# Kernel tuning notes

Measured on AMD Instinct MI355X. Metric: run time of the kernel, lower is better.

The kernel has to match this reference:

```python
import jax, jax.numpy as jnp
import numpy as np
from jax import lax

B = 4096
PRO_VOCAB, PRO_LEN, PRO_K = 25, 1000, 8
LIG_VOCAB, LIG_LEN, LIG_K = 64, 100, 4
CH = 96  # 2*CH = 192 = 6*32 per the reshape in the original forward
DN = ('NCH', 'OIH', 'NCH')  # 1D conv dimension numbers


def setup_inputs() -> dict:
    key = jax.random.key(0)
    ks = jax.random.split(key, 8)
    protein = jax.random.normal(ks[0], (B, PRO_VOCAB, PRO_LEN), dtype=jnp.float32)
    ligand = jax.random.normal(ks[1], (B, LIG_VOCAB, LIG_LEN), dtype=jnp.float32)
    w_pro = jax.random.normal(ks[2], (CH, PRO_VOCAB, PRO_K), dtype=jnp.float32) * 0.05
    b_pro = jnp.zeros((CH,), dtype=jnp.float32)
    w_lig = jax.random.normal(ks[3], (CH, LIG_VOCAB, LIG_K), dtype=jnp.float32) * 0.05
    b_lig = jnp.zeros((CH,), dtype=jnp.float32)
    # QuLinear readout over the 32*32=1024 amplitude-encoded Gram matrix -> scalar
    w_aff = jax.random.normal(ks[4], (1024,), dtype=jnp.float32) * 0.05
    b_aff = jnp.zeros((), dtype=jnp.float32)
    return {"protein": protein, "ligand": ligand, "w_pro": w_pro, "b_pro": b_pro,
            "w_lig": w_lig, "b_lig": b_lig, "w_aff": w_aff, "b_aff": b_aff}


def _conv_branch(x, w, b):
    # Conv1d (valid) -> ReLU -> global max pool over length  =>  (B, CH)
    y = lax.conv_general_dilated(x, w, (1,), 'VALID', dimension_numbers=DN)
    return jnp.max(jax.nn.relu(y + b[None, :, None]), axis=-1)


def reference(protein, ligand, w_pro, b_pro, w_lig, b_lig, w_aff, b_aff):
    x1 = _conv_branch(ligand, w_lig, b_lig)    # (B, 96)
    x2 = _conv_branch(protein, w_pro, b_pro)   # (B, 96)
    x = jnp.concatenate([x1, x2], axis=1).reshape(-1, 6, 32)  # (B, 6, 32)
    # Vectorized per-sample Gram matrix a.T @ a : (B, 32, 32)
    gram = jnp.einsum('bij,bik->bjk', x, x)
    flat = gram.reshape(gram.shape[0], -1)     # (B, 1024)
    # Amplitude encoding: L2-normalize the flattened Gram matrix per sample
    amp = flat / (jnp.linalg.norm(flat, axis=1, keepdims=True) + 1e-12)
    # QuLinear readout -> scalar affinity per sample
    aff = amp @ w_aff + b_aff                  # (B,)
    return aff
```

## Files before the change

### kernel.cpp

```cpp
#include <hip/hip_runtime.h>
#include <math.h>

typedef _Float16 f16;
typedef _Float16 f16x2 __attribute__((ext_vector_type(2)));
typedef _Float16 f16x8 __attribute__((ext_vector_type(8)));
typedef float f32x4 __attribute__((ext_vector_type(4)));

__global__ void repack_pro_kernel(const float* __restrict__ w, f16* __restrict__ wp) {
    constexpr int V = 25, K = 8;
    int i = blockIdx.x * 256 + threadIdx.x;
    if (i >= K * 6 * 64 * 8) return;
    int e = i & 7, l = (i >> 3) & 63, c6 = (i >> 9) % 6, t = i / (512 * 6);
    int r16 = l & 15, g = l >> 4;
    int ch = c6 * 16 + r16, v = g * 8 + e;
    float val = (v < V) ? w[(ch * V + v) * K + t] : 0.f;
    wp[i] = (f16)val;
}

__global__ void repack_lig_kernel(const float* __restrict__ w, f16* __restrict__ wp) {
    constexpr int V = 64, K = 4;
    int i = blockIdx.x * 256 + threadIdx.x;
    if (i >= 8 * 6 * 64 * 8) return;
    int e = i & 7, l = (i >> 3) & 63, c6 = (i >> 9) % 6, tk = i / (512 * 6);
    int t = tk >> 1, ks = tk & 1;
    int r16 = l & 15, g = l >> 4;
    int ch = c6 * 16 + r16, v = ks * 32 + g * 8 + e;
    wp[i] = (f16)w[(ch * V + v) * K + t];
}

__global__ __launch_bounds__(512, 4) void conv_kernel(
    const float* __restrict__ pro,
    const f16*   __restrict__ wpP,
    const float* __restrict__ bP,
    const float* __restrict__ lig,
    const f16*   __restrict__ wpL,
    const float* __restrict__ bL,
    float* __restrict__ feat,
    int B)
{
    __shared__ __align__(16) char s_raw[264 * 80];
    __shared__ __align__(16) f16  s_w[24576];
    __shared__ float s_red[8 * 96];

    const int tid  = threadIdx.x;
    const int wave = tid >> 6;
    const int lane = tid & 63;
    const int g    = lane >> 4;
    const int r16  = lane & 15;

    if ((int)blockIdx.x < B) {
        constexpr int V = 25, L = 1000, KT = 8, LOUT = 993;
        constexpr int CH = 256, NC = 4, BR = 264, RSB = 80;
        constexpr int P4 = BR / 4, NVP = 13, NU = NVP * P4;
        const size_t b = blockIdx.x;
        const float* gs = pro + b * (size_t)(V * L);

        {   const f16x8* wg = (const f16x8*)wpP;
            f16x8* wl = (f16x8*)s_w;
            #pragma unroll
            for (int u = 0; u < 24576 / 8 / 512; ++u)
                wl[u * 512 + tid] = wg[u * 512 + tid];
        }
        for (int row = tid; row < BR; row += 512) {
            const int swz = ((row >> 3) & 3) << 4;
            *(f16x8*)(s_raw + row * RSB + (48 ^ swz)) = (f16x8){};
        }
        __syncthreads();

        float runmax[6];
        #pragma unroll
        for (int c6 = 0; c6 < 6; ++c6) runmax[c6] = -3.0e38f;

        for (int c = 0; c < NC; ++c) {
            if (c) __syncthreads();
            #pragma unroll
            for (int u = 0; u < 2; ++u) {
                const int i = u * 512 + tid;
                if (i < NU) {
                    const int v2 = i / P4, p4 = i - v2 * P4;
                    const int p  = 4 * p4;
                    const int gp = c * CH + p;
                    float4 x0 = {0.f, 0.f, 0.f, 0.f}, x1 = {0.f, 0.f, 0.f, 0.f};
                    if (gp < L) {
                        x0 = *(const float4*)(gs + (size_t)(2 * v2) * L + gp);
                        if (2 * v2 + 1 < V)
                            x1 = *(const float4*)(gs + (size_t)(2 * v2 + 1) * L + gp);
                    }
                    const int pb = 4 * v2;
                    const int slot = pb & 48, sub = pb & 12;
                    const float vx0[4] = {x0.x, x0.y, x0.z, x0.w};
                    const float vx1[4] = {x1.x, x1.y, x1.z, x1.w};
                    #pragma unroll
                    for (int j = 0; j < 4; ++j) {
                        const int row = p + j;
                        const int swz = ((row >> 3) & 3) << 4;
                        f16x2 hv = { (f16)vx0[j], (f16)vx1[j] };
                        *(f16x2*)(s_raw + row * RSB + ((slot ^ swz) + sub)) = hv;
                    }
                }
            }
            __syncthreads();

            f32x4 acc[2][6] = {};
            #pragma unroll 1
            for (int t = 0; t < KT; ++t) {
                f16x8 bf[6];
                #pragma unroll
                for (int c6 = 0; c6 < 6; ++c6)
                    bf[c6] = *(const f16x8*)(s_w + ((t * 6 + c6) * 64 + lane) * 8);
                #pragma unroll
                for (int rt = 0; rt < 2; ++rt) {
                    const int row = wave * 32 + rt * 16 + r16 + t;
                    const int swz = ((row >> 3) & 3) << 4;
                    f16x8 a = *(const f16x8*)(s_raw + row * RSB + ((g * 16) ^ swz));
                    #pragma unroll
                    for (int c6 = 0; c6 < 6; ++c6)
                        acc[rt][c6] = __builtin_amdgcn_mfma_f32_16x16x32_f16(a, bf[c6], acc[rt][c6], 0, 0, 0);
                }
            }
            #pragma unroll
            for (int rt = 0; rt < 2; ++rt) {
                const int pt = c * CH + wave * 32 + rt * 16;
                if (pt + 16 <= LOUT) {
                    #pragma unroll
                    for (int c6 = 0; c6 < 6; ++c6)
                        #pragma unroll
                        for (int i = 0; i < 4; ++i)
                            runmax[c6] = fmaxf(runmax[c6], acc[rt][c6][i]);
                } else {
                    const int p0g = pt + g * 4;
                    #pragma unroll
                    for (int c6 = 0; c6 < 6; ++c6)
                        #pragma unroll
                        for (int i = 0; i < 4; ++i)
                            if (p0g + i < LOUT) runmax[c6] = fmaxf(runmax[c6], acc[rt][c6][i]);
                }
            }
        }

        #pragma unroll
        for (int c6 = 0; c6 < 6; ++c6) {
            runmax[c6] = fmaxf(runmax[c6], __shfl_xor(runmax[c6], 16, 64));
            runmax[c6] = fmaxf(runmax[c6], __shfl_xor(runmax[c6], 32, 64));
        }
        if (lane < 16) {
            #pragma unroll
            for (int c6 = 0; c6 < 6; ++c6)
                s_red[wave * 96 + c6 * 16 + lane] = runmax[c6];
        }
        __syncthreads();
        if (tid < 96) {
            float m = s_red[tid];
            #pragma unroll
            for (int w = 1; w < 8; ++w) m = fmaxf(m, s_red[w * 96 + tid]);
            feat[b * 192 + 96 + tid] = fmaxf(m + bP[tid], 0.f);
        }
    } else {
        constexpr int V = 64, L = 100, KT = 4, LOUT = 97;
        constexpr int BR = 120, RSB = 144;
        constexpr int P4 = BR / 4, NVP = 32, NU = NVP * P4;
        const size_t b = blockIdx.x - B;
        const float* gs = lig + b * (size_t)(V * L);

        {   const f16x8* wg = (const f16x8*)wpL;
            f16x8* wl = (f16x8*)s_w;
            #pragma unroll
            for (int u = 0; u < 24576 / 8 / 512; ++u)
                wl[u * 512 + tid] = wg[u * 512 + tid];
        }
        #pragma unroll
        for (int u = 0; u < 2; ++u) {
            const int i = u * 512 + tid;
            if (i < NU) {
                const int v2 = i / P4, p4 = i - v2 * P4;
                const int p  = 4 * p4;
                float4 x0 = {0.f, 0.f, 0.f, 0.f}, x1 = {0.f, 0.f, 0.f, 0.f};
                if (p < L) {
                    x0 = *(const float4*)(gs + (size_t)(2 * v2) * L + p);
                    x1 = *(const float4*)(gs + (size_t)(2 * v2 + 1) * L + p);
                }
                const int pb = 4 * v2;
                const int slot = pb & 0x70, sub = pb & 12;
                const float vx0[4] = {x0.x, x0.y, x0.z, x0.w};
                const float vx1[4] = {x1.x, x1.y, x1.z, x1.w};
                #pragma unroll
                for (int j = 0; j < 4; ++j) {
                    const int row = p + j;
                    const int swz = ((row >> 3) & 3) << 4;
                    f16x2 hv = { (f16)vx0[j], (f16)vx1[j] };
                    *(f16x2*)(s_raw + row * RSB + ((slot ^ swz) + sub)) = hv;
                }
            }
        }
        __syncthreads();

        if (wave < 7) {
            f32x4 acc[6] = {};
            #pragma unroll 1
            for (int t = 0; t < KT; ++t) {
                #pragma unroll
                for (int ks = 0; ks < 2; ++ks) {
                    f16x8 bf[6];
                    #pragma unroll
                    for (int c6 = 0; c6 < 6; ++c6)
                        bf[c6] = *(const f16x8*)(s_w + (((t * 2 + ks) * 6 + c6) * 64 + lane) * 8);
                    const int row = wave * 16 + r16 + t;
                    const int swz = ((row >> 3) & 3) << 4;
                    f16x8 a = *(const f16x8*)(s_raw + row * RSB + ((ks * 64 + g * 16) ^ swz));
                    #pragma unroll
                    for (int c6 = 0; c6 < 6; ++c6)
                        acc[c6] = __builtin_amdgcn_mfma_f32_16x16x32_f16(a, bf[c6], acc[c6], 0, 0, 0);
                }
            }
            float runmax[6];
            const int p0g = wave * 16 + g * 4;
            #pragma unroll
            for (int c6 = 0; c6 < 6; ++c6) {
                runmax[c6] = -3.0e38f;
                #pragma unroll
                for (int i = 0; i < 4; ++i)
                    if (p0g + i < LOUT) runmax[c6] = fmaxf(runmax[c6], acc[c6][i]);
                runmax[c6] = fmaxf(runmax[c6], __shfl_xor(runmax[c6], 16, 64));
                runmax[c6] = fmaxf(runmax[c6], __shfl_xor(runmax[c6], 32, 64));
            }
            if (lane < 16) {
                #pragma unroll
                for (int c6 = 0; c6 < 6; ++c6)
                    s_red[wave * 96 + c6 * 16 + lane] = runmax[c6];
            }
        }
        __syncthreads();
        if (tid < 96) {
            float m = s_red[tid];
            #pragma unroll
            for (int w = 1; w < 7; ++w) m = fmaxf(m, s_red[w * 96 + tid]);
            feat[b * 192 + tid] = fmaxf(m + bL[tid], 0.f);
        }
    }
}

__global__ __launch_bounds__(256) void gram_affinity_kernel(
    const float* __restrict__ feat, const float* __restrict__ w_aff,
    const float* __restrict__ b_aff, float* __restrict__ out, int B)
{
    const int lane = threadIdx.x & 63;
    const int wid  = threadIdx.x >> 6;
    const int b    = blockIdx.x * 4 + wid;

    __shared__ float s_x[4][192];

    if (b < B) {
        const float* fp = feat + (size_t)b * 192;
        for (int i = lane; i < 192; i += 64) s_x[wid][i] = fp[i];
    }
    __syncthreads();

    if (b < B) {
        float ssum = 0.f, sdot = 0.f;
        #pragma unroll
        for (int t = 0; t < 16; ++t) {
            const int jk = t * 64 + lane;
            const int j = jk >> 5, k = jk & 31;
            float gg = 0.f;
            #pragma unroll
            for (int i = 0; i < 6; ++i)
                gg = fmaf(s_x[wid][i * 32 + j], s_x[wid][i * 32 + k], gg);
            ssum = fmaf(gg, gg, ssum);
            sdot = fmaf(gg, w_aff[jk], sdot);
        }
        #pragma unroll
        for (int off = 32; off >= 1; off >>= 1) {
            ssum += __shfl_xor(ssum, off, 64);
            sdot += __shfl_xor(sdot, off, 64);
        }
        if (lane == 0) out[b] = sdot / (sqrtf(ssum) + 1e-12f) + b_aff[0];
    }
}

extern "C" void kernel_launch(void* const* d_in, const int* in_sizes, int n_in,
                              void* d_out, int out_size, void* d_ws, size_t ws_size,
                              hipStream_t stream)
{
    const float* protein = (const float*)d_in[0];
    const float* ligand  = (const float*)d_in[1];
    const float* w_pro   = (const float*)d_in[2];
    const float* b_pro   = (const float*)d_in[3];
    const float* w_lig   = (const float*)d_in[4];
    const float* b_lig   = (const float*)d_in[5];
    const float* w_aff   = (const float*)d_in[6];
    const float* b_aff   = (const float*)d_in[7];
    float* out = (float*)d_out;
    const int B = out_size;

    float* feat   = (float*)d_ws;
    f16*   wpackP = (f16*)((char*)d_ws + (size_t)B * 192 * 4);
    f16*   wpackL = wpackP + 24576;

    repack_pro_kernel<<<96, 256, 0, stream>>>(w_pro, wpackP);
    repack_lig_kernel<<<96, 256, 0, stream>>>(w_lig, wpackL);

    conv_kernel<<<2 * B, 512, 0, stream>>>(
        protein, wpackP, b_pro, ligand, wpackL, b_lig, feat, B);

    gram_affinity_kernel<<<(B + 3) / 4, 256, 0, stream>>>(feat, w_aff, b_aff, out, B);
}
```

Measured before the change: 249.4 us.

## Stage whole protein sequence in LDS with 1024-thread blocks

Replaces the four-chunk protein loop with a single pass: blocks grow to 1024 threads (16 waves), the full 1032-row fp16 protein tile is staged into LDS at once, and each wave computes four 16-row MFMA tiles. This removes the per-chunk barriers and the repeated staging/compute alternation. In exchange, LDS use per block rises to roughly 133 KB and register pressure per wave grows, which limits blocks per CU. The ligand half, which needs only 7 waves, now launches with 1024 threads, so most of those threads sit idle.

```diff
diff --git a/kernel.cpp b/kernel.cpp
--- a/kernel.cpp
+++ b/kernel.cpp
@@ -28,7 +28,7 @@
     wp[i] = (f16)w[(ch * V + v) * K + t];
 }
 
-__global__ __launch_bounds__(512, 4) void conv_kernel(
+__global__ __launch_bounds__(1024) void conv_kernel(
     const float* __restrict__ pro,
     const f16*   __restrict__ wpP,
     const float* __restrict__ bP,
@@ -38,9 +38,9 @@
     float* __restrict__ feat,
     int B)
 {
-    __shared__ __align__(16) char s_raw[264 * 80];
+    __shared__ __align__(16) char s_raw[1032 * 80];
     __shared__ __align__(16) f16  s_w[24576];
-    __shared__ float s_red[8 * 96];
+    __shared__ float s_red[16 * 96];
 
     const int tid  = threadIdx.x;
     const int wave = tid >> 6;
@@ -50,137 +50,38 @@
 
     if ((int)blockIdx.x < B) {
         constexpr int V = 25, L = 1000, KT = 8, LOUT = 993;
-        constexpr int CH = 256, NC = 4, BR = 264, RSB = 80;
-        constexpr int P4 = BR / 4, NVP = 13, NU = NVP * P4;
+        constexpr int BR = 1032, RSB = 80;
+        constexpr int P4 = BR / 4;
+        constexpr int NU = 13 * P4;
         const size_t b = blockIdx.x;
         const float* gs = pro + b * (size_t)(V * L);
 
         {   const f16x8* wg = (const f16x8*)wpP;
             f16x8* wl = (f16x8*)s_w;
             #pragma unroll
-            for (int u = 0; u < 24576 / 8 / 512; ++u)
-                wl[u * 512 + tid] = wg[u * 512 + tid];
-        }
-        for (int row = tid; row < BR; row += 512) {
+            for (int u = 0; u < 3; ++u)
+                wl[u * 1024 + tid] = wg[u * 1024 + tid];
+        }
+        for (int row = tid; row < BR; row += 1024) {
             const int swz = ((row >> 3) & 3) << 4;
             *(f16x8*)(s_raw + row * RSB + (48 ^ swz)) = (f16x8){};
         }
         __syncthreads();
 
-        float runmax[6];
-        #pragma unroll
-        for (int c6 = 0; c6 < 6; ++c6) runmax[c6] = -3.0e38f;
-
-        for (int c = 0; c < NC; ++c) {
-            if (c) __syncthreads();
-            #pragma unroll
-            for (int u = 0; u < 2; ++u) {
-                const int i = u * 512 + tid;
-                if (i < NU) {
-                    const int v2 = i / P4, p4 = i - v2 * P4;
-                    const int p  = 4 * p4;
-                    const int gp = c * CH + p;
-                    float4 x0 = {0.f, 0.f, 0.f, 0.f}, x1 = {0.f, 0.f, 0.f, 0.f};
-                    if (gp < L) {
-                        x0 = *(const float4*)(gs + (size_t)(2 * v2) * L + gp);
-                        if (2 * v2 + 1 < V)
-                            x1 = *(const float4*)(gs + (size_t)(2 * v2 + 1) * L + gp);
-                    }
-                    const int pb = 4 * v2;
-                    const int slot = pb & 48, sub = pb & 12;
-                    const float vx0[4] = {x0.x, x0.y, x0.z, x0.w};
-                    const float vx1[4] = {x1.x, x1.y, x1.z, x1.w};
-                    #pragma unroll
-                    for (int j = 0; j < 4; ++j) {
-                        const int row = p + j;
-                        const int swz = ((row >> 3) & 3) << 4;
-                        f16x2 hv = { (f16)vx0[j], (f16)vx1[j] };
-                        *(f16x2*)(s_raw + row * RSB + ((slot ^ swz) + sub)) = hv;
-                    }
-                }
-            }
-            __syncthreads();
-
-            f32x4 acc[2][6] = {};
-            #pragma unroll 1
-            for (int t = 0; t < KT; ++t) {
-                f16x8 bf[6];
-                #pragma unroll
-                for (int c6 = 0; c6 < 6; ++c6)
-                    bf[c6] = *(const f16x8*)(s_w + ((t * 6 + c6) * 64 + lane) * 8);
-                #pragma unroll
-                for (int rt = 0; rt < 2; ++rt) {
-                    const int row = wave * 32 + rt * 16 + r16 + t;
-                    const int swz = ((row >> 3) & 3) << 4;
-                    f16x8 a = *(const f16x8*)(s_raw + row * RSB + ((g * 16) ^ swz));
-                    #pragma unroll
-                    for (int c6 = 0; c6 < 6; ++c6)
-                        acc[rt][c6] = __builtin_amdgcn_mfma_f32_16x16x32_f16(a, bf[c6], acc[rt][c6], 0, 0, 0);
-                }
-            }
-            #pragma unroll
-            for (int rt = 0; rt < 2; ++rt) {
-                const int pt = c * CH + wave * 32 + rt * 16;
-                if (pt + 16 <= LOUT) {
-                    #pragma unroll
-                    for (int c6 = 0; c6 < 6; ++c6)
-                        #pragma unroll
-                        for (int i = 0; i < 4; ++i)
-                            runmax[c6] = fmaxf(runmax[c6], acc[rt][c6][i]);
-                } else {
-                    const int p0g = pt + g * 4;
-                    #pragma unroll
-                    for (int c6 = 0; c6 < 6; ++c6)
-                        #pragma unroll
-                        for (int i = 0; i < 4; ++i)
-                            if (p0g + i < LOUT) runmax[c6] = fmaxf(runmax[c6], acc[rt][c6][i]);
-                }
-            }
-        }
-
-        #pragma unroll
-        for (int c6 = 0; c6 < 6; ++c6) {
-            runmax[c6] = fmaxf(runmax[c6], __shfl_xor(runmax[c6], 16, 64));
-            runmax[c6] = fmaxf(runmax[c6], __shfl_xor(runmax[c6], 32, 64));
-        }
-        if (lane < 16) {
-            #pragma unroll
-            for (int c6 = 0; c6 < 6; ++c6)
-                s_red[wave * 96 + c6 * 16 + lane] = runmax[c6];
-        }
-        __syncthreads();
-        if (tid < 96) {
-            float m = s_red[tid];
-            #pragma unroll
-            for (int w = 1; w < 8; ++w) m = fmaxf(m, s_red[w * 96 + tid]);
-            feat[b * 192 + 96 + tid] = fmaxf(m + bP[tid], 0.f);
-        }
-    } else {
-        constexpr int V = 64, L = 100, KT = 4, LOUT = 97;
-        constexpr int BR = 120, RSB = 144;
-        constexpr int P4 = BR / 4, NVP = 32, NU = NVP * P4;
-        const size_t b = blockIdx.x - B;
-        const float* gs = lig + b * (size_t)(V * L);
-
-        {   const f16x8* wg = (const f16x8*)wpL;
-            f16x8* wl = (f16x8*)s_w;
-            #pragma unroll
-            for (int u = 0; u < 24576 / 8 / 512; ++u)
-                wl[u * 512 + tid] = wg[u * 512 + tid];
-        }
-        #pragma unroll
-        for (int u = 0; u < 2; ++u) {
-            const int i = u * 512 + tid;
+        #pragma unroll
+        for (int u = 0; u < 4; ++u) {
+            const int i = u * 1024 + tid;
             if (i < NU) {
                 const int v2 = i / P4, p4 = i - v2 * P4;
                 const int p  = 4 * p4;
                 float4 x0 = {0.f, 0.f, 0.f, 0.f}, x1 = {0.f, 0.f, 0.f, 0.f};
                 if (p < L) {
                     x0 = *(const float4*)(gs + (size_t)(2 * v2) * L + p);
-                    x1 = *(const float4*)(gs + (size_t)(2 * v2 + 1) * L + p);
+                    if (2 * v2 + 1 < V)
+                        x1 = *(const float4*)(gs + (size_t)(2 * v2 + 1) * L + p);
                 }
                 const int pb = 4 * v2;
-                const int slot = pb & 0x70, sub = pb & 12;
+                const int slot = pb & 48, sub = pb & 12;
                 const float vx0[4] = {x0.x, x0.y, x0.z, x0.w};
                 const float vx1[4] = {x1.x, x1.y, x1.z, x1.w};
                 #pragma unroll
@@ -190,6 +91,98 @@
                     f16x2 hv = { (f16)vx0[j], (f16)vx1[j] };
                     *(f16x2*)(s_raw + row * RSB + ((slot ^ swz) + sub)) = hv;
                 }
+            }
+        }
+        __syncthreads();
+
+        float runmax[6];
+        #pragma unroll
+        for (int c6 = 0; c6 < 6; ++c6) runmax[c6] = -3.0e38f;
+
+        f32x4 acc[4][6] = {};
+        #pragma unroll 1
+        for (int t = 0; t < KT; ++t) {
+            f16x8 bf[6];
+            #pragma unroll
+            for (int c6 = 0; c6 < 6; ++c6)
+                bf[c6] = *(const f16x8*)(s_w + ((t * 6 + c6) * 64 + lane) * 8);
+            #pragma unroll
+            for (int rt = 0; rt < 4; ++rt) {
+                const int row = wave * 64 + rt * 16 + r16 + t;
+                const int swz = ((row >> 3) & 3) << 4;
+                f16x8 a = *(const f16x8*)(s_raw + row * RSB + ((g * 16) ^ swz));
+                #pragma unroll
+                for (int c6 = 0; c6 < 6; ++c6)
+                    acc[rt][c6] = __builtin_amdgcn_mfma_f32_16x16x32_f16(a, bf[c6], acc[rt][c6], 0, 0, 0);
+            }
+        }
+        #pragma unroll
+        for (int rt = 0; rt < 4; ++rt) {
+            const int pt = wave * 64 + rt * 16;
+            if (pt + 16 <= LOUT) {
+                #pragma unroll
+                for (int c6 = 0; c6 < 6; ++c6)
+                    #pragma unroll
+                    for (int i = 0; i < 4; ++i)
+                        runmax[c6] = fmaxf(runmax[c6], acc[rt][c6][i]);
+            } else {
+                const int p0g = pt + g * 4;
+                #pragma unroll
+                for (int c6 = 0; c6 < 6; ++c6)
+                    #pragma unroll
+                    for (int i = 0; i < 4; ++i)
+                        if (p0g + i < LOUT) runmax[c6] = fmaxf(runmax[c6], acc[rt][c6][i]);
+            }
+        }
+
+        #pragma unroll
+        for (int c6 = 0; c6 < 6; ++c6) {
+            runmax[c6] = fmaxf(runmax[c6], __shfl_xor(runmax[c6], 16, 64));
+            runmax[c6] = fmaxf(runmax[c6], __shfl_xor(runmax[c6], 32, 64));
+        }
+        if (lane < 16) {
+            #pragma unroll
+            for (int c6 = 0; c6 < 6; ++c6)
+                s_red[wave * 96 + c6 * 16 + lane] = runmax[c6];
+        }
+        __syncthreads();
+        if (tid < 96) {
+            float m = s_red[tid];
+            #pragma unroll
+            for (int w = 1; w < 16; ++w) m = fmaxf(m, s_red[w * 96 + tid]);
+            feat[b * 192 + 96 + tid] = fmaxf(m + bP[tid], 0.f);
+        }
+    } else {
+        constexpr int V = 64, L = 100, KT = 4, LOUT = 97;
+        constexpr int BR = 120, RSB = 144;
+        constexpr int P4 = BR / 4, NU = 32 * P4;
+        const size_t b = blockIdx.x - B;
+        const float* gs = lig + b * (size_t)(V * L);
+
+        {   const f16x8* wg = (const f16x8*)wpL;
+            f16x8* wl = (f16x8*)s_w;
+            #pragma unroll
+            for (int u = 0; u < 3; ++u)
+                wl[u * 1024 + tid] = wg[u * 1024 + tid];
+        }
+        if (tid < NU) {
+            const int v2 = tid / P4, p4 = tid - v2 * P4;
+            const int p  = 4 * p4;
+            float4 x0 = {0.f, 0.f, 0.f, 0.f}, x1 = {0.f, 0.f, 0.f, 0.f};
+            if (p < L) {
+                x0 = *(const float4*)(gs + (size_t)(2 * v2) * L + p);
+                x1 = *(const float4*)(gs + (size_t)(2 * v2 + 1) * L + p);
+            }
+            const int pb = 4 * v2;
+            const int slot = pb & 0x70, sub = pb & 12;
+            const float vx0[4] = {x0.x, x0.y, x0.z, x0.w};
+            const float vx1[4] = {x1.x, x1.y, x1.z, x1.w};
+            #pragma unroll
+            for (int j = 0; j < 4; ++j) {
+                const int row = p + j;
+                const int swz = ((row >> 3) & 3) << 4;
+                f16x2 hv = { (f16)vx0[j], (f16)vx1[j] };
+                *(f16x2*)(s_raw + row * RSB + ((slot ^ swz) + sub)) = hv;
             }
         }
         __syncthreads();
@@ -299,7 +292,7 @@
     repack_pro_kernel<<<96, 256, 0, stream>>>(w_pro, wpackP);
     repack_lig_kernel<<<96, 256, 0, stream>>>(w_lig, wpackL);
 
-    conv_kernel<<<2 * B, 512, 0, stream>>>(
+    conv_kernel<<<2 * B, 1024, 0, stream>>>(
         protein, wpackP, b_pro, ligand, wpackL, b_lig, feat, B);
 
     gram_affinity_kernel<<<(B + 3) / 4, 256, 0, stream>>>(feat, w_aff, b_aff, out, B);
```

Result: slower. 422.5 us (+69.4%).

## Split protein conv MFMA tile across row and channel waves, widen staging loads

Applied to the files above, without the earlier changes.

The protein branch now uses a 4x2 wave grid: each wave covers 64 output positions and 3 of the 6 channel groups, instead of 32 positions and all 6 groups. This halves the B-fragment loads per wave and doubles the reuse of each A fragment, while keeping the same number of MFMAs per wave. Input staging also changes so each thread loads four vocab rows at once and writes f16x4 to LDS, using one pass of 462 threads instead of two passes of 858 items. The cross-wave max reduction is adjusted to match the new split.

```diff
diff --git a/kernel.cpp b/kernel.cpp
--- a/kernel.cpp
+++ b/kernel.cpp
@@ -3,6 +3,7 @@
 
 typedef _Float16 f16;
 typedef _Float16 f16x2 __attribute__((ext_vector_type(2)));
+typedef _Float16 f16x4 __attribute__((ext_vector_type(4)));
 typedef _Float16 f16x8 __attribute__((ext_vector_type(8)));
 typedef float f32x4 __attribute__((ext_vector_type(4)));
 
@@ -51,9 +52,11 @@
     if ((int)blockIdx.x < B) {
         constexpr int V = 25, L = 1000, KT = 8, LOUT = 993;
         constexpr int CH = 256, NC = 4, BR = 264, RSB = 80;
-        constexpr int P4 = BR / 4, NVP = 13, NU = NVP * P4;
+        constexpr int P4 = BR / 4;
+        constexpr int NU = 7 * P4;
         const size_t b = blockIdx.x;
         const float* gs = pro + b * (size_t)(V * L);
+        const int rw = wave & 3, cw = wave >> 2;
 
         {   const f16x8* wg = (const f16x8*)wpP;
             f16x8* wl = (f16x8*)s_w;
@@ -67,98 +70,101 @@
         }
         __syncthreads();
 
-        float runmax[6];
-        #pragma unroll
-        for (int c6 = 0; c6 < 6; ++c6) runmax[c6] = -3.0e38f;
+        float runmax[3];
+        #pragma unroll
+        for (int c3 = 0; c3 < 3; ++c3) runmax[c3] = -3.0e38f;
 
         for (int c = 0; c < NC; ++c) {
             if (c) __syncthreads();
-            #pragma unroll
-            for (int u = 0; u < 2; ++u) {
-                const int i = u * 512 + tid;
-                if (i < NU) {
-                    const int v2 = i / P4, p4 = i - v2 * P4;
-                    const int p  = 4 * p4;
-                    const int gp = c * CH + p;
-                    float4 x0 = {0.f, 0.f, 0.f, 0.f}, x1 = {0.f, 0.f, 0.f, 0.f};
-                    if (gp < L) {
-                        x0 = *(const float4*)(gs + (size_t)(2 * v2) * L + gp);
-                        if (2 * v2 + 1 < V)
-                            x1 = *(const float4*)(gs + (size_t)(2 * v2 + 1) * L + gp);
+            if (tid < NU) {
+                const int vq = tid / P4, p4 = tid - vq * P4;
+                const int p = 4 * p4, gp = c * CH + p;
+                float4 x0 = {0.f,0.f,0.f,0.f}, x1 = {0.f,0.f,0.f,0.f};
+                float4 x2 = {0.f,0.f,0.f,0.f}, x3 = {0.f,0.f,0.f,0.f};
+                if (gp < L) {
+                    x0 = *(const float4*)(gs + (size_t)(4 * vq) * L + gp);
+                    if (vq < 6) {
+                        x1 = *(const float4*)(gs + (size_t)(4 * vq + 1) * L + gp);
+                        x2 = *(const float4*)(gs + (size_t)(4 * vq + 2) * L + gp);
+                        x3 = *(const float4*)(gs + (size_t)(4 * vq + 3) * L + gp);
                     }
-                    const int pb = 4 * v2;
-                    const int slot = pb & 48, sub = pb & 12;
-                    const float vx0[4] = {x0.x, x0.y, x0.z, x0.w};
-                    const float vx1[4] = {x1.x, x1.y, x1.z, x1.w};
-                    #pragma unroll
-                    for (int j = 0; j < 4; ++j) {
-                        const int row = p + j;
-                        const int swz = ((row >> 3) & 3) << 4;
-                        f16x2 hv = { (f16)vx0[j], (f16)vx1[j] };
-                        *(f16x2*)(s_raw + row * RSB + ((slot ^ swz) + sub)) = hv;
-                    }
+                }
+                const int pb = 8 * vq;
+                const int slot = pb & 48, sub = pb & 8;
+                const float a0[4] = {x0.x, x0.y, x0.z, x0.w};
+                const float a1[4] = {x1.x, x1.y, x1.z, x1.w};
+                const float a2[4] = {x2.x, x2.y, x2.z, x2.w};
+                const float a3[4] = {x3.x, x3.y, x3.z, x3.w};
+                #pragma unroll
+                for (int j = 0; j < 4; ++j) {
+                    const int row = p + j;
+                    const int swz = ((row >> 3) & 3) << 4;
+                    f16x4 hv = { (f16)a0[j], (f16)a1[j], (f16)a2[j], (f16)a3[j] };
+                    *(f16x4*)(s_raw + row * RSB + ((slot ^ swz) + sub)) = hv;
                 }
             }
             __syncthreads();
 
-            f32x4 acc[2][6] = {};
+            f32x4 acc[4][3] = {};
             #pragma unroll 1
             for (int t = 0; t < KT; ++t) {
-                f16x8 bf[6];
-                #pragma unroll
-                for (int c6 = 0; c6 < 6; ++c6)
-                    bf[c6] = *(const f16x8*)(s_w + ((t * 6 + c6) * 64 + lane) * 8);
-                #pragma unroll
-                for (int rt = 0; rt < 2; ++rt) {
-                    const int row = wave * 32 + rt * 16 + r16 + t;
+                f16x8 bf[3];
+                #pragma unroll
+                for (int c3 = 0; c3 < 3; ++c3)
+                    bf[c3] = *(const f16x8*)(s_w + ((t * 6 + cw * 3 + c3) * 64 + lane) * 8);
+                #pragma unroll
+                for (int rt = 0; rt < 4; ++rt) {
+                    const int row = rw * 64 + rt * 16 + r16 + t;
                     const int swz = ((row >> 3) & 3) << 4;
                     f16x8 a = *(const f16x8*)(s_raw + row * RSB + ((g * 16) ^ swz));
                     #pragma unroll
-                    for (int c6 = 0; c6 < 6; ++c6)
-                        acc[rt][c6] = __builtin_amdgcn_mfma_f32_16x16x32_f16(a, bf[c6], acc[rt][c6], 0, 0, 0);
-                }
-            }
-            #pragma unroll
-            for (int rt = 0; rt < 2; ++rt) {
-                const int pt = c * CH + wave * 32 + rt * 16;
+                    for (int c3 = 0; c3 < 3; ++c3)
+                        acc[rt][c3] = __builtin_amdgcn_mfma_f32_16x16x32_f16(a, bf[c3], acc[rt][c3], 0, 0, 0);
+                }
+            }
+            #pragma unroll
+            for (int rt = 0; rt < 4; ++rt) {
+                const int pt = c * CH + rw * 64 + rt * 16;
                 if (pt + 16 <= LOUT) {
                     #pragma unroll
-                    for (int c6 = 0; c6 < 6; ++c6)
+                    for (int c3 = 0; c3 < 3; ++c3)
                         #pragma unroll
                         for (int i = 0; i < 4; ++i)
-                            runmax[c6] = fmaxf(runmax[c6], acc[rt][c6][i]);
+                            runmax[c3] = fmaxf(runmax[c3], acc[rt][c3][i]);
                 } else {
                     const int p0g = pt + g * 4;
                     #pragma unroll
-                    for (int c6 = 0; c6 < 6; ++c6)
+                    for (int c3 = 0; c3 < 3; ++c3)
                         #pragma unroll
                         for (int i = 0; i < 4; ++i)
-                            if (p0g + i < LOUT) runmax[c6] = fmaxf(runmax[c6], acc[rt][c6][i]);
-                }
-            }
-        }
-
-        #pragma unroll
-        for (int c6 = 0; c6 < 6; ++c6) {
-            runmax[c6] = fmaxf(runmax[c6], __shfl_xor(runmax[c6], 16, 64));
-            runmax[c6] = fmaxf(runmax[c6], __shfl_xor(runmax[c6], 32, 64));
+                            if (p0g + i < LOUT) runmax[c3] = fmaxf(runmax[c3], acc[rt][c3][i]);
+                }
+            }
+        }
+
+        #pragma unroll
+        for (int c3 = 0; c3 < 3; ++c3) {
+            runmax[c3] = fmaxf(runmax[c3], __shfl_xor(runmax[c3], 16, 64));
+            runmax[c3] = fmaxf(runmax[c3], __shfl_xor(runmax[c3], 32, 64));
         }
         if (lane < 16) {
             #pragma unroll
-            for (int c6 = 0; c6 < 6; ++c6)
-                s_red[wave * 96 + c6 * 16 + lane] = runmax[c6];
+            for (int c3 = 0; c3 < 3; ++c3)
+                s_red[wave * 48 + c3 * 16 + lane] = runmax[c3];
         }
         __syncthreads();
         if (tid < 96) {
-            float m = s_red[tid];
-            #pragma unroll
-            for (int w = 1; w < 8; ++w) m = fmaxf(m, s_red[w * 96 + tid]);
+            const int cw2 = tid / 48, chs = tid - cw2 * 48;
+            float m = s_red[(cw2 * 4) * 48 + chs];
+            #pragma unroll
+            for (int rw2 = 1; rw2 < 4; ++rw2)
+                m = fmaxf(m, s_red[(cw2 * 4 + rw2) * 48 + chs]);
             feat[b * 192 + 96 + tid] = fmaxf(m + bP[tid], 0.f);
         }
     } else {
         constexpr int V = 64, L = 100, KT = 4, LOUT = 97;
         constexpr int BR = 120, RSB = 144;
-        constexpr int P4 = BR / 4, NVP = 32, NU = NVP * P4;
+        constexpr int P4 = BR / 4, NU = 32 * P4;
         const size_t b = blockIdx.x - B;
         const float* gs = lig + b * (size_t)(V * L);
 
```

Result: no change. 245.2 us, median of 2 (-1.7%).
